# Optimization experiments

Measured on AMD Instinct MI355X. Metric: run time of the kernel, lower is better.

The kernel has to match this reference:

```python
import jax, jax.numpy as jnp
import numpy as np


def setup_inputs() -> dict:
    key = jax.random.key(0)
    k = jax.random.split(key, 5)
    bs, n_heads, ch, n_obj, emb = 4, 8, 64, 8, 64
    ih = iw = 32
    T = ih * iw
    return {
        "qkv": jax.random.normal(k[0], (bs, 3 * n_heads * ch, T), dtype=jnp.float32),
        "bboxes": jax.random.uniform(k[1], (bs, n_obj, 5), dtype=jnp.float32),
        "null_prompt_emb": jax.random.normal(k[2], (bs, emb, T), dtype=jnp.float32),
        "prompt_emb": jax.random.normal(k[3], (bs, emb, T), dtype=jnp.float32),
        "W_prompt": jax.random.normal(k[4], (3 * n_heads * ch, emb), dtype=jnp.float32) * 0.02,
        "n_heads": n_heads,
        "image_h": ih,
        "image_w": iw,
    }


def _region_masks(bboxes, h, w):
    # Faithful translation of get_region: bbox unpacked as (x, y, width, height, obj_idx).
    # Returns float masks [b, n_obj, h*w].
    x, y, bw, bh = bboxes[..., 0], bboxes[..., 1], bboxes[..., 2], bboxes[..., 3]
    i0 = jnp.minimum(float(h) - 1.0, jnp.floor(y * h))
    j0 = jnp.minimum(float(w) - 1.0, jnp.floor(x * w))
    i1 = i0 + jnp.maximum(1.0, jnp.ceil(bh * h))
    j1 = j0 + jnp.maximum(1.0, jnp.ceil(bw * w))
    ii = jnp.arange(h, dtype=jnp.float32)
    jj = jnp.arange(w, dtype=jnp.float32)
    mi = (ii >= i0[..., None]) & (ii < i1[..., None])          # [b, n, h]
    mj = (jj >= j0[..., None]) & (jj < j1[..., None])          # [b, n, w]
    m = (mi[..., :, None] & mj[..., None, :]).astype(jnp.float32)  # [b, n, h, w]
    return m.reshape(m.shape[0], m.shape[1], h * w)


def reference(qkv, bboxes, null_prompt_emb, prompt_emb, W_prompt, n_heads, image_h, image_w):
    bs, width, T = qkv.shape
    ch = width // (3 * n_heads)
    scale = float(ch) ** -0.25  # 1/sqrt(sqrt(ch))

    def split3(x):
        x = x.reshape(bs * n_heads, 3 * ch, T)
        return x[:, :ch], x[:, ch:2 * ch], x[:, 2 * ch:]

    q, k, v = split3(qkv)
    # to_prompt_token is a 1x1 Conv1d (no bias) == matmul over the channel dim
    nq, nk, nv = split3(jnp.einsum('oc,bct->bot', W_prompt, null_prompt_emb))
    pq, pk, pv = split3(jnp.einsum('oc,bct->bot', W_prompt, prompt_emb))

    def attn(qh, kh, vh, col_mask=None):
        w = jnp.einsum('bct,bcs->bts', qh * scale, kh * scale)
        if col_mask is not None:
            w = jnp.where(col_mask[:, None, :] > 0.5, w, -1e9)
        w = jax.nn.softmax(w.astype(jnp.float32), axis=-1).astype(qh.dtype)
        return jnp.einsum('bts,bcs->btc', w, vh)  # [bs*heads, T, ch]

    # global (null-prompt) attention
    a_null = attn(q + nq, k + nk, v + nv)

    # per-object masked attention, blended by region masks
    masks = _region_masks(bboxes, image_h, image_w)       # [bs, n_obj, T]
    masks = jnp.repeat(masks, n_heads, axis=0)            # [(bs*heads), n_obj, T]
    qf, kf, vf = q + pq, k + pk, v + pv
    a_fg = jnp.zeros_like(a_null)
    counter = jnp.zeros((bs * n_heads, T, 1), dtype=jnp.float32)
    for o in range(masks.shape[1]):  # small fixed loop over objects
        m = masks[:, o]                                   # [bs*heads, T]
        a_fg = a_fg + m[:, :, None] * attn(qf, kf, vf, col_mask=m)
        counter = counter + m[:, :, None]
    fg = counter > 0.5
    a_final = jnp.where(fg, a_fg, a_null) / jnp.where(fg, counter, 1.0)
    return jnp.transpose(a_final, (0, 2, 1)).reshape(bs, n_heads * ch, T)
```

## Files before the change

kernel.cpp:

```cpp
#include <hip/hip_runtime.h>

#define BS 4
#define NH 8
#define TT 1024
#define WROWS 1536
#define NOBJ 8
#define NT 65536

#define QNT_OFF  0
#define KNT_OFF  2097152
#define VNCS_OFF 4194304
#define QFT_OFF  6291456
#define KFT_OFF  8388608
#define VFT_OFF  10485760

typedef __attribute__((ext_vector_type(8))) short short8;
typedef __attribute__((ext_vector_type(4))) float v4f;

__device__ __forceinline__ short f2bf(float f) {
    unsigned u = __float_as_uint(f);
    u = (u + 0x7FFF + ((u >> 16) & 1)) >> 16;
    return (short)u;
}
__device__ __forceinline__ unsigned cvtpk(float a, float b) {
    unsigned u;
    asm("v_cvt_pk_bf16_f32 %0, %1, %2" : "=v"(u) : "v"(a), "v"(b));
    return u;
}
__device__ __forceinline__ float fexp2(float x) {
    float r;
    asm("v_exp_f32 %0, %1" : "=v"(r) : "v"(x));
    return r;
}
__device__ __forceinline__ int pi64(int s) { return 4 * (s & 15) + (s >> 4); }

__device__ __forceinline__ void get_region(const float* __restrict__ bb,
                                           int& i0, int& j0, int& hh, int& ww) {
    float x = bb[0], y = bb[1], bw = bb[2], bh = bb[3];
    float i0f = fminf(31.0f, floorf(y * 32.0f));
    float j0f = fminf(31.0f, floorf(x * 32.0f));
    float i1f = i0f + fmaxf(1.0f, ceilf(bh * 32.0f));
    float j1f = j0f + fmaxf(1.0f, ceilf(bw * 32.0f));
    i0 = (int)i0f; j0 = (int)j0f;
    int i1 = min(32, (int)i1f);
    int j1 = min(32, (int)j1f);
    hh = i1 - i0; ww = j1 - j0;
}

__global__ __launch_bounds__(256)
void fuse_kernel(const float* __restrict__ qkv, const float* __restrict__ nEmb,
                 const float* __restrict__ pEmb, const float* __restrict__ W,
                 short* __restrict__ wsS) {
    __shared__ __align__(16) short Ent[64 * 72];
    __shared__ __align__(16) short Ept[64 * 72];
    __shared__ __align__(16) short sbuf[64 * 72];
    int t0 = blockIdx.x * 64;
    int r0 = blockIdx.y * 64;
    int b  = blockIdx.z;
    int tid = threadIdx.x;
    int w = tid >> 6, lane = tid & 63, ln = lane & 15, qd = lane >> 4;

    {
        int e  = tid >> 4;
        int t4 = (tid & 15) * 4;
#pragma unroll
        for (int p = 0; p < 4; ++p) {
            int ee = p * 16 + e;
            float4 n4 = *(const float4*)&nEmb[(b * 64 + ee) * TT + t0 + t4];
            float4 p4 = *(const float4*)&pEmb[(b * 64 + ee) * TT + t0 + t4];
            Ent[(t4 + 0) * 72 + ee] = f2bf(n4.x); Ent[(t4 + 1) * 72 + ee] = f2bf(n4.y);
            Ent[(t4 + 2) * 72 + ee] = f2bf(n4.z); Ent[(t4 + 3) * 72 + ee] = f2bf(n4.w);
            Ept[(t4 + 0) * 72 + ee] = f2bf(p4.x); Ept[(t4 + 1) * 72 + ee] = f2bf(p4.y);
            Ept[(t4 + 2) * 72 + ee] = f2bf(p4.z); Ept[(t4 + 3) * 72 + ee] = f2bf(p4.w);
        }
    }
    short8 aw0, aw1;
    {
        const float* wp = &W[(r0 + 16 * w + ln) * 64 + qd * 8];
        float4 f0 = *(const float4*)wp;
        float4 f1 = *(const float4*)(wp + 4);
        float4 f2 = *(const float4*)(wp + 32);
        float4 f3 = *(const float4*)(wp + 36);
        uint4 u0, u1;
        u0.x = cvtpk(f0.x, f0.y); u0.y = cvtpk(f0.z, f0.w);
        u0.z = cvtpk(f1.x, f1.y); u0.w = cvtpk(f1.z, f1.w);
        u1.x = cvtpk(f2.x, f2.y); u1.y = cvtpk(f2.z, f2.w);
        u1.z = cvtpk(f3.x, f3.y); u1.w = cvtpk(f3.z, f3.w);
        aw0 = *(short8*)&u0; aw1 = *(short8*)&u1;
    }
    __syncthreads();
    v4f accN[4], accP[4];
#pragma unroll
    for (int nn = 0; nn < 4; ++nn) {
        const short* bp = &Ent[(nn * 16 + ln) * 72 + qd * 8];
        short8 b0 = *(const short8*)bp;
        short8 b1 = *(const short8*)(bp + 32);
        v4f z = (v4f){0.f, 0.f, 0.f, 0.f};
        z = __builtin_amdgcn_mfma_f32_16x16x32_bf16(aw0, b0, z, 0, 0, 0);
        z = __builtin_amdgcn_mfma_f32_16x16x32_bf16(aw1, b1, z, 0, 0, 0);
        accN[nn] = z;
        const short* cp = &Ept[(nn * 16 + ln) * 72 + qd * 8];
        short8 c0 = *(const short8*)cp;
        short8 c1 = *(const short8*)(cp + 32);
        v4f y = (v4f){0.f, 0.f, 0.f, 0.f};
        y = __builtin_amdgcn_mfma_f32_16x16x32_bf16(aw0, c0, y, 0, 0, 0);
        y = __builtin_amdgcn_mfma_f32_16x16x32_bf16(aw1, c1, y, 0, 0, 0);
        accP[nn] = y;
    }
    int sec = (r0 % 192) / 64;
    int h = r0 / 192, bh = b * 8 + h;
    float sc = (sec == 0) ? 0.18033688f : 1.0f;
    float xan[4][4], xap[4][4];
#pragma unroll
    for (int nn = 0; nn < 4; ++nn)
#pragma unroll
        for (int i = 0; i < 4; ++i) {
            int r = r0 + 16 * w + 4 * qd + i;
            float x = qkv[(b * WROWS + r) * TT + t0 + nn * 16 + ln];
            xan[nn][i] = (accN[nn][i] + x) * sc;
            xap[nn][i] = (accP[nn][i] + x) * sc;
        }

    if (sec == 2) {
        short* Vn = wsS + VNCS_OFF + bh * NT;
        __syncthreads();
#pragma unroll
        for (int nn = 0; nn < 4; ++nn)
#pragma unroll
            for (int i = 0; i < 4; ++i)
                sbuf[(16 * w + 4 * qd + i) * 72 + 4 * ln + nn] = f2bf(xan[nn][i]);
        __syncthreads();
#pragma unroll
        for (int rep = 0; rep < 2; ++rep) {
            int idx = rep * 256 + tid; int cl = idx >> 3, c8 = idx & 7;
            *(short8*)&Vn[cl * TT + t0 + c8 * 8] = *(const short8*)&sbuf[cl * 72 + c8 * 8];
        }
        __syncthreads();
        short* dst = wsS + VFT_OFF + bh * NT + t0 * 64;
#pragma unroll
        for (int nn = 0; nn < 4; ++nn) {
            uint2 u; u.x = cvtpk(xap[nn][0], xap[nn][1]); u.y = cvtpk(xap[nn][2], xap[nn][3]);
            *(uint2*)&sbuf[(nn * 16 + ln) * 72 + 16 * w + 4 * qd] = u;
        }
        __syncthreads();
#pragma unroll
        for (int rep = 0; rep < 2; ++rep) {
            int idx = rep * 256 + tid; int tl = idx >> 3, c8 = idx & 7;
            *(short8*)&dst[tl * 64 + c8 * 8] = *(const short8*)&sbuf[tl * 72 + c8 * 8];
        }
    } else {
        short* dn = wsS + (sec == 0 ? QNT_OFF : KNT_OFF) + bh * NT + t0 * 64;
        short* df = wsS + (sec == 0 ? QFT_OFF : KFT_OFF) + bh * NT + t0 * 64;
        __syncthreads();
#pragma unroll
        for (int nn = 0; nn < 4; ++nn) {
            uint2 u; u.x = cvtpk(xan[nn][0], xan[nn][1]); u.y = cvtpk(xan[nn][2], xan[nn][3]);
            *(uint2*)&sbuf[(nn * 16 + ln) * 72 + 16 * w + 4 * qd] = u;
        }
        __syncthreads();
#pragma unroll
        for (int rep = 0; rep < 2; ++rep) {
            int idx = rep * 256 + tid; int tl = idx >> 3, c8 = idx & 7;
            *(short8*)&dn[tl * 64 + c8 * 8] = *(const short8*)&sbuf[tl * 72 + c8 * 8];
        }
        __syncthreads();
#pragma unroll
        for (int nn = 0; nn < 4; ++nn) {
            uint2 u; u.x = cvtpk(xap[nn][0], xap[nn][1]); u.y = cvtpk(xap[nn][2], xap[nn][3]);
            *(uint2*)&sbuf[(nn * 16 + ln) * 72 + 16 * w + 4 * qd] = u;
        }
        __syncthreads();
#pragma unroll
        for (int rep = 0; rep < 2; ++rep) {
            int idx = rep * 256 + tid; int tl = idx >> 3, c8 = idx & 7;
            *(short8*)&df[tl * 64 + c8 * 8] = *(const short8*)&sbuf[tl * 72 + c8 * 8];
        }
    }
}

__global__ __launch_bounds__(256)
void attn_fused(const short* __restrict__ wsS, const float* __restrict__ bboxes,
                float* __restrict__ out) {
    __shared__ __align__(16) short lds[23040];
    __shared__ unsigned short tmap[1024];
    short* Qs  = lds;
    short* Kb0 = lds + 4608;
    short* Kb1 = lds + 9216;
    short* Vb0 = lds + 13824;
    short* Vb1 = lds + 18432;
    int bh = blockIdx.x, rt = blockIdx.y;
    int b = bh >> 3, h = bh & 7;
    int t0 = rt * 64;
    int tid = threadIdx.x;
    int w = tid >> 6, lane = tid & 63, ln = lane & 15, qd = lane >> 4;
    const short* QnT = wsS + QNT_OFF + bh * NT;
    const short* KnT = wsS + KNT_OFF + bh * NT;
    const short* Vn  = wsS + VNCS_OFF + bh * NT;
    const short* QfT = wsS + QFT_OFF + bh * NT;
    const short* KfT = wsS + KFT_OFF + bh * NT;
    const short* VfT = wsS + VFT_OFF + bh * NT;
    int sidx = tid, scell = sidx >> 3, sc8 = sidx & 7;
    int sidx2 = 256 + tid, scell2 = sidx2 >> 3, sc82 = sidx2 & 7;

    *(short8*)&Qs[scell * 72 + sc8 * 8]  = *(const short8*)&QnT[(t0 + scell) * 64 + sc8 * 8];
    *(short8*)&Qs[scell2 * 72 + sc82 * 8] = *(const short8*)&QnT[(t0 + scell2) * 64 + sc82 * 8];
    __syncthreads();
    short8 aq0 = *(const short8*)&Qs[(16 * w + ln) * 72 + qd * 8];
    short8 aq1 = *(const short8*)&Qs[(16 * w + ln) * 72 + 32 + qd * 8];
    v4f O[4]; float l[4];
#pragma unroll
    for (int r = 0; r < 4; ++r) l[r] = 0.f;
#pragma unroll
    for (int cc = 0; cc < 4; ++cc) O[cc] = (v4f){0.f, 0.f, 0.f, 0.f};
    short8 kreg[2], vreg[2];
    kreg[0] = *(const short8*)&KnT[scell * 64 + sc8 * 8];
    kreg[1] = *(const short8*)&KnT[scell2 * 64 + sc82 * 8];
    vreg[0] = *(const short8*)&Vn[scell * TT + sc8 * 8];
    vreg[1] = *(const short8*)&Vn[scell2 * TT + sc82 * 8];
    *(short8*)&Kb0[scell * 72 + sc8 * 8]  = kreg[0];
    *(short8*)&Kb0[scell2 * 72 + sc82 * 8] = kreg[1];
    *(short8*)&Vb0[scell * 72 + sc8 * 8]  = vreg[0];
    *(short8*)&Vb0[scell2 * 72 + sc82 * 8] = vreg[1];
    kreg[0] = *(const short8*)&KnT[(64 + scell) * 64 + sc8 * 8];
    kreg[1] = *(const short8*)&KnT[(64 + scell2) * 64 + sc82 * 8];
    vreg[0] = *(const short8*)&Vn[scell * TT + 64 + sc8 * 8];
    vreg[1] = *(const short8*)&Vn[scell2 * TT + 64 + sc82 * 8];
    __syncthreads();
    for (int ct = 0; ct < 16; ++ct) {
        const short* Kc = (ct & 1) ? Kb1 : Kb0;
        const short* Vc = (ct & 1) ? Vb1 : Vb0;
        short* Kn_ = (ct & 1) ? Kb0 : Kb1;
        short* Vn_ = (ct & 1) ? Vb0 : Vb1;
        if (ct < 15) {
            *(short8*)&Kn_[scell * 72 + sc8 * 8]  = kreg[0];
            *(short8*)&Kn_[scell2 * 72 + sc82 * 8] = kreg[1];
            *(short8*)&Vn_[scell * 72 + sc8 * 8]  = vreg[0];
            *(short8*)&Vn_[scell2 * 72 + sc82 * 8] = vreg[1];
        }
        if (ct < 14) {
            int s0 = (ct + 2) * 64;
            kreg[0] = *(const short8*)&KnT[(s0 + scell) * 64 + sc8 * 8];
            kreg[1] = *(const short8*)&KnT[(s0 + scell2) * 64 + sc82 * 8];
            vreg[0] = *(const short8*)&Vn[scell * TT + s0 + sc8 * 8];
            vreg[1] = *(const short8*)&Vn[scell2 * TT + s0 + sc82 * 8];
        }
        v4f S[4];
#pragma unroll
        for (int nn = 0; nn < 4; ++nn) {
            short8 b0 = *(const short8*)&Kc[(nn * 16 + ln) * 72 + qd * 8];
            short8 b1 = *(const short8*)&Kc[(nn * 16 + ln) * 72 + 32 + qd * 8];
            v4f z = (v4f){0.f, 0.f, 0.f, 0.f};
            z = __builtin_amdgcn_mfma_f32_16x16x32_bf16(aq0, b0, z, 0, 0, 0);
            z = __builtin_amdgcn_mfma_f32_16x16x32_bf16(aq1, b1, z, 0, 0, 0);
            S[nn] = z;
        }
#pragma unroll
        for (int r = 0; r < 4; ++r) {
            float e0 = fexp2(S[0][r]);
            float e1 = fexp2(S[1][r]);
            float e2 = fexp2(S[2][r]);
            float e3 = fexp2(S[3][r]);
            l[r] += (e0 + e1) + (e2 + e3);
            uint2 u; u.x = cvtpk(e0, e1); u.y = cvtpk(e2, e3);
            *(uint2*)&Qs[(w * 16 + 4 * qd + r) * 72 + 4 * ln] = u;
        }
        short8 ap0 = *(const short8*)&Qs[(w * 16 + ln) * 72 + qd * 8];
        short8 ap1 = *(const short8*)&Qs[(w * 16 + ln) * 72 + 32 + qd * 8];
#pragma unroll
        for (int cc = 0; cc < 4; ++cc) {
            short8 bv0 = *(const short8*)&Vc[(cc * 16 + ln) * 72 + qd * 8];
            short8 bv1 = *(const short8*)&Vc[(cc * 16 + ln) * 72 + 32 + qd * 8];
            O[cc] = __builtin_amdgcn_mfma_f32_16x16x32_bf16(ap0, bv0, O[cc], 0, 0, 0);
            O[cc] = __builtin_amdgcn_mfma_f32_16x16x32_bf16(ap1, bv1, O[cc], 0, 0, 0);
        }
        __syncthreads();
    }
    v4f Onull[4];
#pragma unroll
    for (int r = 0; r < 4; ++r) {
        float rs = l[r];
        rs += __shfl_xor(rs, 1, 64);
        rs += __shfl_xor(rs, 2, 64);
        rs += __shfl_xor(rs, 4, 64);
        rs += __shfl_xor(rs, 8, 64);
        float inv = 1.0f / rs;
#pragma unroll
        for (int cc = 0; cc < 4; ++cc) Onull[cc][r] = O[cc][r] * inv;
    }

    *(short8*)&Qs[scell * 72 + sc8 * 8]  = *(const short8*)&QfT[(t0 + scell) * 64 + sc8 * 8];
    *(short8*)&Qs[scell2 * 72 + sc82 * 8] = *(const short8*)&QfT[(t0 + scell2) * 64 + sc82 * 8];
    __syncthreads();
    aq0 = *(const short8*)&Qs[(16 * w + ln) * 72 + qd * 8];
    aq1 = *(const short8*)&Qs[(16 * w + ln) * 72 + 32 + qd * 8];
    v4f Oacc[4]; float cnt[4];
#pragma unroll
    for (int r = 0; r < 4; ++r) cnt[r] = 0.f;
#pragma unroll
    for (int cc = 0; cc < 4; ++cc) Oacc[cc] = (v4f){0.f, 0.f, 0.f, 0.f};
    int pA = pi64(scell), pB = pi64(scell2);

    for (int o = 0; o < NOBJ; ++o) {
        int i0, j0, hh, ww;
        get_region(&bboxes[(b * NOBJ + o) * 5], i0, j0, hh, ww);
        int i1 = i0 + hh;
        if (i0 > 2 * rt + 1 || i1 <= 2 * rt) continue;
        int R = hh * ww;
        for (int idx = tid; idx < R; idx += 256) {
            int ri = idx / ww; int rj = idx - ri * ww;
            tmap[idx] = (unsigned short)((i0 + ri) * 32 + j0 + rj);
        }
        __syncthreads();
#pragma unroll
        for (int r = 0; r < 4; ++r) l[r] = 0.f;
#pragma unroll
        for (int cc = 0; cc < 4; ++cc) O[cc] = (v4f){0.f, 0.f, 0.f, 0.f};
        int nct = (R + 63) >> 6;
        {
            int tA = tmap[min(scell, R - 1)];
            int tB = tmap[min(scell2, R - 1)];
            kreg[0] = *(const short8*)&KfT[tA * 64 + sc8 * 8];
            kreg[1] = *(const short8*)&KfT[tB * 64 + sc82 * 8];
            vreg[0] = *(const short8*)&VfT[tA * 64 + sc8 * 8];
            vreg[1] = *(const short8*)&VfT[tB * 64 + sc82 * 8];
        }
        *(short8*)&Kb0[scell * 72 + sc8 * 8]  = kreg[0];
        *(short8*)&Kb0[scell2 * 72 + sc82 * 8] = kreg[1];
#pragma unroll
        for (int jj = 0; jj < 8; ++jj) {
            int j = (jj + sc8) & 7;
            Vb0[(sc8 * 8 + j) * 72 + pA] = vreg[0][j];
        }
#pragma unroll
        for (int jj = 0; jj < 8; ++jj) {
            int j = (jj + sc82) & 7;
            Vb0[(sc82 * 8 + j) * 72 + pB] = vreg[1][j];
        }
        if (nct > 1) {
            int tA = tmap[min(64 + scell, R - 1)];
            int tB = tmap[min(64 + scell2, R - 1)];
            kreg[0] = *(const short8*)&KfT[tA * 64 + sc8 * 8];
            kreg[1] = *(const short8*)&KfT[tB * 64 + sc82 * 8];
            vreg[0] = *(const short8*)&VfT[tA * 64 + sc8 * 8];
            vreg[1] = *(const short8*)&VfT[tB * 64 + sc82 * 8];
        }
        __syncthreads();
        for (int ct = 0; ct < nct; ++ct) {
            int sb = ct * 64;
            const short* Kc = (ct & 1) ? Kb1 : Kb0;
            const short* Vc = (ct & 1) ? Vb1 : Vb0;
            short* Kn_ = (ct & 1) ? Kb0 : Kb1;
            short* Vn_ = (ct & 1) ? Vb0 : Vb1;
            if (ct + 1 < nct) {
                *(short8*)&Kn_[scell * 72 + sc8 * 8]  = kreg[0];
                *(short8*)&Kn_[scell2 * 72 + sc82 * 8] = kreg[1];
#pragma unroll
                for (int jj = 0; jj < 8; ++jj) {
                    int j = (jj + sc8) & 7;
                    Vn_[(sc8 * 8 + j) * 72 + pA] = vreg[0][j];
                }
#pragma unroll
                for (int jj = 0; jj < 8; ++jj) {
                    int j = (jj + sc82) & 7;
                    Vn_[(sc82 * 8 + j) * 72 + pB] = vreg[1][j];
                }
            }
            if (ct + 2 < nct) {
                int s0 = sb + 128;
                int tA = tmap[min(s0 + scell, R - 1)];
                int tB = tmap[min(s0 + scell2, R - 1)];
                kreg[0] = *(const short8*)&KfT[tA * 64 + sc8 * 8];
                kreg[1] = *(const short8*)&KfT[tB * 64 + sc82 * 8];
                vreg[0] = *(const short8*)&VfT[tA * 64 + sc8 * 8];
                vreg[1] = *(const short8*)&VfT[tB * 64 + sc82 * 8];
            }
            v4f S[4];
#pragma unroll
            for (int nn = 0; nn < 4; ++nn) {
                short8 b0 = *(const short8*)&Kc[(nn * 16 + ln) * 72 + qd * 8];
                short8 b1 = *(const short8*)&Kc[(nn * 16 + ln) * 72 + 32 + qd * 8];
                v4f z = (v4f){0.f, 0.f, 0.f, 0.f};
                z = __builtin_amdgcn_mfma_f32_16x16x32_bf16(aq0, b0, z, 0, 0, 0);
                z = __builtin_amdgcn_mfma_f32_16x16x32_bf16(aq1, b1, z, 0, 0, 0);
                S[nn] = z;
            }
            float v0 = (sb +  0 + ln) < R ? 1.f : 0.f;
            float v1 = (sb + 16 + ln) < R ? 1.f : 0.f;
            float v2 = (sb + 32 + ln) < R ? 1.f : 0.f;
            float v3 = (sb + 48 + ln) < R ? 1.f : 0.f;
#pragma unroll
            for (int r = 0; r < 4; ++r) {
                float e0 = fexp2(S[0][r]) * v0;
                float e1 = fexp2(S[1][r]) * v1;
                float e2 = fexp2(S[2][r]) * v2;
                float e3 = fexp2(S[3][r]) * v3;
                l[r] += (e0 + e1) + (e2 + e3);
                uint2 u; u.x = cvtpk(e0, e1); u.y = cvtpk(e2, e3);
                *(uint2*)&Qs[(w * 16 + 4 * qd + r) * 72 + 4 * ln] = u;
            }
            short8 ap0 = *(const short8*)&Qs[(w * 16 + ln) * 72 + qd * 8];
            short8 ap1 = *(const short8*)&Qs[(w * 16 + ln) * 72 + 32 + qd * 8];
#pragma unroll
            for (int cc = 0; cc < 4; ++cc) {
                short8 bv0 = *(const short8*)&Vc[(cc * 16 + ln) * 72 + qd * 8];
                short8 bv1 = *(const short8*)&Vc[(cc * 16 + ln) * 72 + 32 + qd * 8];
                O[cc] = __builtin_amdgcn_mfma_f32_16x16x32_bf16(ap0, bv0, O[cc], 0, 0, 0);
                O[cc] = __builtin_amdgcn_mfma_f32_16x16x32_bf16(ap1, bv1, O[cc], 0, 0, 0);
            }
            __syncthreads();
        }
#pragma unroll
        for (int r = 0; r < 4; ++r) {
            float rs = l[r];
            rs += __shfl_xor(rs, 1, 64);
            rs += __shfl_xor(rs, 2, 64);
            rs += __shfl_xor(rs, 4, 64);
            rs += __shfl_xor(rs, 8, 64);
            float inv = 1.0f / rs;
            int t = t0 + 16 * w + 4 * qd + r;
            int ti = t >> 5, tj = t & 31;
            bool in = (ti >= i0) && (ti < i1) && (tj >= j0) && (tj < j0 + ww);
            if (in) {
                cnt[r] += 1.f;
#pragma unroll
                for (int cc = 0; cc < 4; ++cc) Oacc[cc][r] += O[cc][r] * inv;
            }
        }
    }

    __syncthreads();
    float* Ot = (float*)lds;
#pragma unroll
    for (int r = 0; r < 4; ++r) {
        int tl = 16 * w + 4 * qd + r;
        float icnt = cnt[r] > 0.f ? 1.0f / cnt[r] : 0.f;
#pragma unroll
        for (int cc = 0; cc < 4; ++cc) {
            float val = cnt[r] > 0.f ? Oacc[cc][r] * icnt : Onull[cc][r];
            Ot[(cc * 16 + ln) * 68 + tl] = val;
        }
    }
    __syncthreads();
    int obase = (b * 512 + h * 64) * TT + t0;
#pragma unroll
    for (int rep = 0; rep < 4; ++rep) {
        int idx = rep * 256 + tid; int c = idx >> 4, t4 = (idx & 15) * 4;
        *(float4*)&out[obase + c * TT + t4] = *(float4*)&Ot[c * 68 + t4];
    }
}

extern "C" void kernel_launch(void* const* d_in, const int* in_sizes, int n_in,
                              void* d_out, int out_size, void* d_ws, size_t ws_size,
                              hipStream_t stream) {
    const float* qkv    = (const float*)d_in[0];
    const float* bboxes = (const float*)d_in[1];
    const float* nEmb   = (const float*)d_in[2];
    const float* pEmb   = (const float*)d_in[3];
    const float* W      = (const float*)d_in[4];
    short* wsS = (short*)d_ws;
    float* out = (float*)d_out;

    fuse_kernel<<<dim3(16, 24, 4), 256, 0, stream>>>(qkv, nEmb, pEmb, W, wsS);
    attn_fused<<<dim3(32, 16), 256, 0, stream>>>(wsS, bboxes, out);
}
```

Measured before the change: 148.9 us.

## Compute S transposed so P stays in registers, dropping LDS round-trip

```diff
diff --git a/kernel.cpp b/kernel.cpp
--- a/kernel.cpp
+++ b/kernel.cpp
@@ -32,7 +32,9 @@
     asm("v_exp_f32 %0, %1" : "=v"(r) : "v"(x));
     return r;
 }
-__device__ __forceinline__ int pi64(int s) { return 4 * (s & 15) + (s >> 4); }
+__device__ __forceinline__ int piP(int s) {
+    return 32 * (s >> 5) + 8 * ((s >> 2) & 3) + 4 * ((s >> 4) & 1) + (s & 3);
+}
 
 __device__ __forceinline__ void get_region(const float* __restrict__ bb,
                                            int& i0, int& j0, int& hh, int& ww) {
@@ -125,10 +127,12 @@
         short* Vn = wsS + VNCS_OFF + bh * NT;
         __syncthreads();
 #pragma unroll
-        for (int nn = 0; nn < 4; ++nn)
+        for (int nn = 0; nn < 4; ++nn) {
+            int colb = 32 * (nn >> 1) + 4 * (nn & 1) + 8 * (ln >> 2) + (ln & 3);
 #pragma unroll
             for (int i = 0; i < 4; ++i)
-                sbuf[(16 * w + 4 * qd + i) * 72 + 4 * ln + nn] = f2bf(xan[nn][i]);
+                sbuf[(16 * w + 4 * qd + i) * 72 + colb] = f2bf(xan[nn][i]);
+        }
         __syncthreads();
 #pragma unroll
         for (int rep = 0; rep < 2; ++rep) {
@@ -181,13 +185,13 @@
 __global__ __launch_bounds__(256)
 void attn_fused(const short* __restrict__ wsS, const float* __restrict__ bboxes,
                 float* __restrict__ out) {
-    __shared__ __align__(16) short lds[23040];
+    __shared__ __align__(16) short lds[18432];
     __shared__ unsigned short tmap[1024];
-    short* Qs  = lds;
-    short* Kb0 = lds + 4608;
-    short* Kb1 = lds + 9216;
-    short* Vb0 = lds + 13824;
-    short* Vb1 = lds + 18432;
+    short* Kb0 = lds;
+    short* Kb1 = lds + 4608;
+    short* Vb0 = lds + 9216;
+    short* Vb1 = lds + 13824;
+    float* Ot  = (float*)lds;
     int bh = blockIdx.x, rt = blockIdx.y;
     int b = bh >> 3, h = bh & 7;
     int t0 = rt * 64;
@@ -202,14 +206,9 @@
     int sidx = tid, scell = sidx >> 3, sc8 = sidx & 7;
     int sidx2 = 256 + tid, scell2 = sidx2 >> 3, sc82 = sidx2 & 7;
 
-    *(short8*)&Qs[scell * 72 + sc8 * 8]  = *(const short8*)&QnT[(t0 + scell) * 64 + sc8 * 8];
-    *(short8*)&Qs[scell2 * 72 + sc82 * 8] = *(const short8*)&QnT[(t0 + scell2) * 64 + sc82 * 8];
-    __syncthreads();
-    short8 aq0 = *(const short8*)&Qs[(16 * w + ln) * 72 + qd * 8];
-    short8 aq1 = *(const short8*)&Qs[(16 * w + ln) * 72 + 32 + qd * 8];
-    v4f O[4]; float l[4];
-#pragma unroll
-    for (int r = 0; r < 4; ++r) l[r] = 0.f;
+    short8 aq0 = *(const short8*)&QnT[(t0 + 16 * w + ln) * 64 + qd * 8];
+    short8 aq1 = *(const short8*)&QnT[(t0 + 16 * w + ln) * 64 + 32 + qd * 8];
+    v4f O[4]; float l = 0.f;
 #pragma unroll
     for (int cc = 0; cc < 4; ++cc) O[cc] = (v4f){0.f, 0.f, 0.f, 0.f};
     short8 kreg[2], vreg[2];
@@ -247,25 +246,27 @@
         v4f S[4];
 #pragma unroll
         for (int nn = 0; nn < 4; ++nn) {
-            short8 b0 = *(const short8*)&Kc[(nn * 16 + ln) * 72 + qd * 8];
-            short8 b1 = *(const short8*)&Kc[(nn * 16 + ln) * 72 + 32 + qd * 8];
+            short8 k0 = *(const short8*)&Kc[(nn * 16 + ln) * 72 + qd * 8];
+            short8 k1 = *(const short8*)&Kc[(nn * 16 + ln) * 72 + 32 + qd * 8];
             v4f z = (v4f){0.f, 0.f, 0.f, 0.f};
-            z = __builtin_amdgcn_mfma_f32_16x16x32_bf16(aq0, b0, z, 0, 0, 0);
-            z = __builtin_amdgcn_mfma_f32_16x16x32_bf16(aq1, b1, z, 0, 0, 0);
+            z = __builtin_amdgcn_mfma_f32_16x16x32_bf16(k0, aq0, z, 0, 0, 0);
+            z = __builtin_amdgcn_mfma_f32_16x16x32_bf16(k1, aq1, z, 0, 0, 0);
             S[nn] = z;
         }
-#pragma unroll
-        for (int r = 0; r < 4; ++r) {
-            float e0 = fexp2(S[0][r]);
-            float e1 = fexp2(S[1][r]);
-            float e2 = fexp2(S[2][r]);
-            float e3 = fexp2(S[3][r]);
-            l[r] += (e0 + e1) + (e2 + e3);
-            uint2 u; u.x = cvtpk(e0, e1); u.y = cvtpk(e2, e3);
-            *(uint2*)&Qs[(w * 16 + 4 * qd + r) * 72 + 4 * ln] = u;
-        }
-        short8 ap0 = *(const short8*)&Qs[(w * 16 + ln) * 72 + qd * 8];
-        short8 ap1 = *(const short8*)&Qs[(w * 16 + ln) * 72 + 32 + qd * 8];
+        float p[4][4];
+#pragma unroll
+        for (int nn = 0; nn < 4; ++nn)
+#pragma unroll
+            for (int r = 0; r < 4; ++r) {
+                p[nn][r] = fexp2(S[nn][r]);
+                l += p[nn][r];
+            }
+        uint4 ua, ub;
+        ua.x = cvtpk(p[0][0], p[0][1]); ua.y = cvtpk(p[0][2], p[0][3]);
+        ua.z = cvtpk(p[1][0], p[1][1]); ua.w = cvtpk(p[1][2], p[1][3]);
+        ub.x = cvtpk(p[2][0], p[2][1]); ub.y = cvtpk(p[2][2], p[2][3]);
+        ub.z = cvtpk(p[3][0], p[3][1]); ub.w = cvtpk(p[3][2], p[3][3]);
+        short8 ap0 = *(short8*)&ua, ap1 = *(short8*)&ub;
 #pragma unroll
         for (int cc = 0; cc < 4; ++cc) {
             short8 bv0 = *(const short8*)&Vc[(cc * 16 + ln) * 72 + qd * 8];
@@ -276,29 +277,26 @@
         __syncthreads();
     }
     v4f Onull[4];
-#pragma unroll
-    for (int r = 0; r < 4; ++r) {
-        float rs = l[r];
-        rs += __shfl_xor(rs, 1, 64);
-        rs += __shfl_xor(rs, 2, 64);
-        rs += __shfl_xor(rs, 4, 64);
-        rs += __shfl_xor(rs, 8, 64);
-        float inv = 1.0f / rs;
-#pragma unroll
-        for (int cc = 0; cc < 4; ++cc) Onull[cc][r] = O[cc][r] * inv;
-    }
-
-    *(short8*)&Qs[scell * 72 + sc8 * 8]  = *(const short8*)&QfT[(t0 + scell) * 64 + sc8 * 8];
-    *(short8*)&Qs[scell2 * 72 + sc82 * 8] = *(const short8*)&QfT[(t0 + scell2) * 64 + sc82 * 8];
-    __syncthreads();
-    aq0 = *(const short8*)&Qs[(16 * w + ln) * 72 + qd * 8];
-    aq1 = *(const short8*)&Qs[(16 * w + ln) * 72 + 32 + qd * 8];
+    {
+        float rs = l;
+        rs += __shfl_xor(rs, 16, 64);
+        rs += __shfl_xor(rs, 32, 64);
+#pragma unroll
+        for (int r = 0; r < 4; ++r) {
+            float inv = 1.0f / __shfl(rs, 4 * qd + r, 64);
+#pragma unroll
+            for (int cc = 0; cc < 4; ++cc) Onull[cc][r] = O[cc][r] * inv;
+        }
+    }
+
+    aq0 = *(const short8*)&QfT[(t0 + 16 * w + ln) * 64 + qd * 8];
+    aq1 = *(const short8*)&QfT[(t0 + 16 * w + ln) * 64 + 32 + qd * 8];
     v4f Oacc[4]; float cnt[4];
 #pragma unroll
     for (int r = 0; r < 4; ++r) cnt[r] = 0.f;
 #pragma unroll
     for (int cc = 0; cc < 4; ++cc) Oacc[cc] = (v4f){0.f, 0.f, 0.f, 0.f};
-    int pA = pi64(scell), pB = pi64(scell2);
+    int pA = piP(scell), pB = piP(scell2);
 
     for (int o = 0; o < NOBJ; ++o) {
         int i0, j0, hh, ww;
@@ -311,8 +309,7 @@
             tmap[idx] = (unsigned short)((i0 + ri) * 32 + j0 + rj);
         }
         __syncthreads();
-#pragma unroll
-        for (int r = 0; r < 4; ++r) l[r] = 0.f;
+        l = 0.f;
 #pragma unroll
         for (int cc = 0; cc < 4; ++cc) O[cc] = (v4f){0.f, 0.f, 0.f, 0.f};
         int nct = (R + 63) >> 6;
@@ -377,29 +374,29 @@
             v4f S[4];
 #pragma unroll
             for (int nn = 0; nn < 4; ++nn) {
-                short8 b0 = *(const short8*)&Kc[(nn * 16 + ln) * 72 + qd * 8];
-                short8 b1 = *(const short8*)&Kc[(nn * 16 + ln) * 72 + 32 + qd * 8];
+                short8 k0 = *(const short8*)&Kc[(nn * 16 + ln) * 72 + qd * 8];
+                short8 k1 = *(const short8*)&Kc[(nn * 16 + ln) * 72 + 32 + qd * 8];
                 v4f z = (v4f){0.f, 0.f, 0.f, 0.f};
-                z = __builtin_amdgcn_mfma_f32_16x16x32_bf16(aq0, b0, z, 0, 0, 0);
-                z = __builtin_amdgcn_mfma_f32_16x16x32_bf16(aq1, b1, z, 0, 0, 0);
+                z = __builtin_amdgcn_mfma_f32_16x16x32_bf16(k0, aq0, z, 0, 0, 0);
+                z = __builtin_amdgcn_mfma_f32_16x16x32_bf16(k1, aq1, z, 0, 0, 0);
                 S[nn] = z;
             }
-            float v0 = (sb +  0 + ln) < R ? 1.f : 0.f;
-            float v1 = (sb + 16 + ln) < R ? 1.f : 0.f;
-            float v2 = (sb + 32 + ln) < R ? 1.f : 0.f;
-            float v3 = (sb + 48 + ln) < R ? 1.f : 0.f;
-#pragma unroll
-            for (int r = 0; r < 4; ++r) {
-                float e0 = fexp2(S[0][r]) * v0;
-                float e1 = fexp2(S[1][r]) * v1;
-                float e2 = fexp2(S[2][r]) * v2;
-                float e3 = fexp2(S[3][r]) * v3;
-                l[r] += (e0 + e1) + (e2 + e3);
-                uint2 u; u.x = cvtpk(e0, e1); u.y = cvtpk(e2, e3);
-                *(uint2*)&Qs[(w * 16 + 4 * qd + r) * 72 + 4 * ln] = u;
-            }
-            short8 ap0 = *(const short8*)&Qs[(w * 16 + ln) * 72 + qd * 8];
-            short8 ap1 = *(const short8*)&Qs[(w * 16 + ln) * 72 + 32 + qd * 8];
+            float p[4][4];
+            int sbase = sb + 4 * qd;
+#pragma unroll
+            for (int nn = 0; nn < 4; ++nn)
+#pragma unroll
+                for (int r = 0; r < 4; ++r) {
+                    float vm = (sbase + 16 * nn + r) < R ? 1.f : 0.f;
+                    p[nn][r] = fexp2(S[nn][r]) * vm;
+                    l += p[nn][r];
+                }
+            uint4 ua, ub;
+            ua.x = cvtpk(p[0][0], p[0][1]); ua.y = cvtpk(p[0][2], p[0][3]);
+            ua.z = cvtpk(p[1][0], p[1][1]); ua.w = cvtpk(p[1][2], p[1][3]);
+            ub.x = cvtpk(p[2][0], p[2][1]); ub.y = cvtpk(p[2][2], p[2][3]);
+            ub.z = cvtpk(p[3][0], p[3][1]); ub.w = cvtpk(p[3][2], p[3][3]);
+            short8 ap0 = *(short8*)&ua, ap1 = *(short8*)&ub;
 #pragma unroll
             for (int cc = 0; cc < 4; ++cc) {
                 short8 bv0 = *(const short8*)&Vc[(cc * 16 + ln) * 72 + qd * 8];
@@ -409,27 +406,26 @@
             }
             __syncthreads();
         }
-#pragma unroll
-        for (int r = 0; r < 4; ++r) {
-            float rs = l[r];
-            rs += __shfl_xor(rs, 1, 64);
-            rs += __shfl_xor(rs, 2, 64);
-            rs += __shfl_xor(rs, 4, 64);
-            rs += __shfl_xor(rs, 8, 64);
-            float inv = 1.0f / rs;
-            int t = t0 + 16 * w + 4 * qd + r;
-            int ti = t >> 5, tj = t & 31;
-            bool in = (ti >= i0) && (ti < i1) && (tj >= j0) && (tj < j0 + ww);
-            if (in) {
-                cnt[r] += 1.f;
-#pragma unroll
-                for (int cc = 0; cc < 4; ++cc) Oacc[cc][r] += O[cc][r] * inv;
+        {
+            float rs = l;
+            rs += __shfl_xor(rs, 16, 64);
+            rs += __shfl_xor(rs, 32, 64);
+#pragma unroll
+            for (int r = 0; r < 4; ++r) {
+                float inv = 1.0f / __shfl(rs, 4 * qd + r, 64);
+                int t = t0 + 16 * w + 4 * qd + r;
+                int ti = t >> 5, tj = t & 31;
+                bool in = (ti >= i0) && (ti < i1) && (tj >= j0) && (tj < j0 + ww);
+                if (in) {
+                    cnt[r] += 1.f;
+#pragma unroll
+                    for (int cc = 0; cc < 4; ++cc) Oacc[cc][r] += O[cc][r] * inv;
+                }
             }
         }
     }
 
     __syncthreads();
-    float* Ot = (float*)lds;
 #pragma unroll
     for (int r = 0; r < 4; ++r) {
         int tl = 16 * w + 4 * qd + r;
```

Measured after the change: 143.5 us (median of 2 runs). 3.6% less time.
